# Kernel optimization log

Hardware: AMD Instinct MI355X
Metric: run time of the kernel (lower is better)

Reference implementation:

```python
import jax, jax.numpy as jnp
import numpy as np

N = 100000      # nodes
E = 3200000     # edges (avg degree 32)
IN = 256        # in_channels
OUT = 8         # out_channels
H1, C1 = 4, 4   # conv1: heads=4, out_channels=4 (concat -> 16)


def setup_inputs() -> dict:
    key = jax.random.key(0)
    ks = jax.random.split(key, 10)
    x = jax.random.normal(ks[0], (N, IN), jnp.float32)
    edge_index = jax.random.randint(ks[1], (2, E), 0, N, dtype=jnp.int64)

    def glorot(k, shape):
        fan_in = shape[0]
        return jax.random.normal(k, shape, jnp.float32) / np.float32(np.sqrt(fan_in))

    W1l = glorot(ks[2], (IN, H1 * C1))
    W1r = glorot(ks[3], (IN, H1 * C1))
    a1 = jax.random.normal(ks[4], (H1, C1), jnp.float32) / np.float32(np.sqrt(C1))
    b1 = jnp.zeros((H1 * C1,), jnp.float32)
    W2l = glorot(ks[5], (H1 * C1, OUT))
    W2r = glorot(ks[6], (H1 * C1, OUT))
    a2 = jax.random.normal(ks[7], (1, OUT), jnp.float32) / np.float32(np.sqrt(OUT))
    b2 = jnp.zeros((OUT,), jnp.float32)
    return {"x": x, "edge_index": edge_index, "W1l": W1l, "W1r": W1r, "a1": a1,
            "b1": b1, "W2l": W2l, "W2r": W2r, "a2": a2, "b2": b2}


def gatv2_conv(x, edge_index, Wl, Wr, att, bias, heads, ch, concat):
    # GATv2: e_ij = a^T LeakyReLU(Wl x_j + Wr x_i), softmax over incoming edges of i
    n = x.shape[0]
    src, dst = edge_index[0], edge_index[1]          # message flows src -> dst
    xl = (x @ Wl).reshape(n, heads, ch)              # [N,H,C] (source transform)
    xr = (x @ Wr).reshape(n, heads, ch)              # [N,H,C] (target transform)
    e = jax.nn.leaky_relu(xl[src] + xr[dst], 0.2)    # [E,H,C]
    logits = jnp.einsum('ehc,hc->eh', e, att)        # [E,H]
    # segment softmax over dst (stable: subtract per-target max)
    m = jax.ops.segment_max(logits, dst, num_segments=n)          # [N,H]
    ex = jnp.exp(logits - m[dst])                                  # [E,H]
    denom = jax.ops.segment_sum(ex, dst, num_segments=n)          # [N,H]
    alpha = ex / (denom[dst] + 1e-16)                              # [E,H]
    out = jax.ops.segment_sum(alpha[:, :, None] * xl[src], dst, num_segments=n)  # [N,H,C]
    out = out.reshape(n, heads * ch) if concat else out.mean(axis=1)
    return out + bias


def reference(x, edge_index, W1l, W1r, a1, b1, W2l, W2r, a2, b2):
    # eval mode: feature/attention dropout (p=0.6) are identity
    h = jax.nn.elu(gatv2_conv(x, edge_index, W1l, W1r, a1, b1, H1, C1, True))
    h = gatv2_conv(h, edge_index, W2l, W2r, a2, b2, 1, OUT, False)
    return jax.nn.sigmoid(h)
```

## Files before the change

kernel.cpp:

```cpp
#include <hip/hip_runtime.h>
#include <math.h>

#define NN 100000
#define NE 3200000
#define BW 512
#define BSH 9
#define NB 196
#define EPB_A 8192
#define NBLK_A ((NE + EPB_A - 1) / EPB_A)

__device__ __forceinline__ float lrelu(float v) { return v >= 0.f ? v : 0.2f * v; }


__global__ __launch_bounds__(256) void k_bhist(const int* __restrict__ dst,
                                               unsigned* __restrict__ btot) {
  __shared__ unsigned lh[NB];
  int tid = threadIdx.x;
  if (tid < NB) lh[tid] = 0;
  __syncthreads();
  int base = blockIdx.x * EPB_A;
  int end = min(base + EPB_A, NE);
  for (int e = base + tid * 4; e < end; e += 1024) {
    int4 d4 = *(const int4*)(dst + e);
    atomicAdd(&lh[((unsigned)d4.x) >> BSH], 1u);
    atomicAdd(&lh[((unsigned)d4.y) >> BSH], 1u);
    atomicAdd(&lh[((unsigned)d4.z) >> BSH], 1u);
    atomicAdd(&lh[((unsigned)d4.w) >> BSH], 1u);
  }
  __syncthreads();
  if (tid < NB && lh[tid]) atomicAdd(&btot[tid], lh[tid]);
}

__global__ __launch_bounds__(256) void k_bscan(const unsigned* __restrict__ btot,
    unsigned* __restrict__ bstart, unsigned* __restrict__ bcur) {
  __shared__ unsigned sm[256];
  int tid = threadIdx.x;
  unsigned v = (tid < NB) ? btot[tid] : 0;
  sm[tid] = v;
  __syncthreads();
  for (int off = 1; off < 256; off <<= 1) {
    unsigned u = (tid >= off) ? sm[tid - off] : 0;
    __syncthreads();
    sm[tid] += u;
    __syncthreads();
  }
  unsigned exc = sm[tid] - v;
  if (tid < NB) { bstart[tid] = exc; bcur[tid] = exc; }
  if (tid == NB - 1) bstart[NB] = sm[tid];
}

__global__ __launch_bounds__(256) void k_bin(const int* __restrict__ src,
    const int* __restrict__ dst, unsigned* __restrict__ bcur,
    unsigned* __restrict__ abuf) {
  __shared__ unsigned lh[NB], gb[NB], lcur[NB];
  int tid = threadIdx.x;
  if (tid < NB) lh[tid] = 0;
  __syncthreads();
  int base = blockIdx.x * EPB_A;
  int end = min(base + EPB_A, NE);
  for (int e = base + tid * 4; e < end; e += 1024) {
    int4 d4 = *(const int4*)(dst + e);
    atomicAdd(&lh[((unsigned)d4.x) >> BSH], 1u);
    atomicAdd(&lh[((unsigned)d4.y) >> BSH], 1u);
    atomicAdd(&lh[((unsigned)d4.z) >> BSH], 1u);
    atomicAdd(&lh[((unsigned)d4.w) >> BSH], 1u);
  }
  __syncthreads();
  if (tid < NB) {
    unsigned c = lh[tid];
    gb[tid] = c ? atomicAdd(&bcur[tid], c) : 0u;
    lcur[tid] = 0;
  }
  __syncthreads();
  for (int e = base + tid * 4; e < end; e += 1024) {
    int4 d4 = *(const int4*)(dst + e);
    int4 s4 = *(const int4*)(src + e);
    #pragma unroll
    for (int k = 0; k < 4; ++k) {
      unsigned d = (unsigned)(&d4.x)[k];
      unsigned s = (unsigned)(&s4.x)[k];
      unsigned b = d >> BSH;
      unsigned p = gb[b] + atomicAdd(&lcur[b], 1u);
      abuf[p] = ((d & (BW - 1)) << 17) | s;
    }
  }
}

__global__ __launch_bounds__(256) void k_bsort(const unsigned* __restrict__ bstart,
    const unsigned* __restrict__ abuf, int* __restrict__ rowstart,
    int* __restrict__ cnt, int* __restrict__ ssrc) {
  __shared__ unsigned lh[BW];
  __shared__ unsigned lcur[BW];
  __shared__ unsigned sm[256];
  int b = blockIdx.x, tid = threadIdx.x;
  unsigned s0 = bstart[b], s1 = bstart[b + 1];
  lh[tid] = 0; lh[tid + 256] = 0;
  __syncthreads();
  for (unsigned i = s0 + tid; i < s1; i += 256)
    atomicAdd(&lh[abuf[i] >> 17], 1u);
  __syncthreads();
  unsigned a0 = lh[2 * tid], a1 = lh[2 * tid + 1];
  sm[tid] = a0 + a1;
  __syncthreads();
  for (int off = 1; off < 256; off <<= 1) {
    unsigned u = (tid >= off) ? sm[tid - off] : 0;
    __syncthreads();
    sm[tid] += u;
    __syncthreads();
  }
  unsigned exc = sm[tid] - (a0 + a1);
  int node = b * BW + 2 * tid;
  if (node < NN)     { rowstart[node]     = s0 + exc;      cnt[node]     = a0; }
  if (node + 1 < NN) { rowstart[node + 1] = s0 + exc + a0; cnt[node + 1] = a1; }
  lcur[2 * tid] = exc;
  lcur[2 * tid + 1] = exc + a0;
  __syncthreads();
  for (unsigned i = s0 + tid; i < s1; i += 256) {
    unsigned v = abuf[i];
    unsigned p = s0 + atomicAdd(&lcur[v >> 17], 1u);
    ssrc[p] = (int)(v & 0x1FFFFu);
  }
}


__global__ __launch_bounds__(256) void k1_lin1(const float* __restrict__ x,
    const float* __restrict__ W1l, const float* __restrict__ W1r,
    float* __restrict__ xl1, float* __restrict__ xr1) {
  __shared__ float lw[256][32];
  int tid = threadIdx.x;
  for (int i = tid; i < 256 * 16; i += 256) {
    int k = i >> 4, c = i & 15;
    lw[k][c]      = W1l[i];
    lw[k][16 + c] = W1r[i];
  }
  __syncthreads();
  int row = blockIdx.x * 256 + tid;
  if (row >= NN) return;
  const float4* xr4 = (const float4*)(x + (size_t)row * 256);

  float acc[32];
  #pragma unroll
  for (int c = 0; c < 32; ++c) acc[c] = 0.f;

  float4 va = xr4[0], vb = xr4[1];
  for (int k4 = 0; k4 < 64; k4 += 2) {
    float4 vc = xr4[(k4 + 2) & 63];
    float4 vd = xr4[(k4 + 3) & 63];
    #pragma unroll
    for (int half = 0; half < 2; ++half) {
      float4 v = half ? vb : va;
      int kb = (k4 + half) * 4;
      #pragma unroll
      for (int kk = 0; kk < 4; ++kk) {
        float xk = (&v.x)[kk];
        const float4* wrow = (const float4*)&lw[kb + kk][0];
        #pragma unroll
        for (int q = 0; q < 8; ++q) {
          float4 w = wrow[q];
          acc[q * 4 + 0] = fmaf(xk, w.x, acc[q * 4 + 0]);
          acc[q * 4 + 1] = fmaf(xk, w.y, acc[q * 4 + 1]);
          acc[q * 4 + 2] = fmaf(xk, w.z, acc[q * 4 + 2]);
          acc[q * 4 + 3] = fmaf(xk, w.w, acc[q * 4 + 3]);
        }
      }
    }
    va = vc; vb = vd;
  }
  float4* ol = (float4*)(xl1 + (size_t)row * 16);
  float4* orr = (float4*)(xr1 + (size_t)row * 16);
  #pragma unroll
  for (int q = 0; q < 4; ++q) {
    ol[q]  = make_float4(acc[q*4+0], acc[q*4+1], acc[q*4+2], acc[q*4+3]);
    orr[q] = make_float4(acc[16+q*4+0], acc[16+q*4+1], acc[16+q*4+2], acc[16+q*4+3]);
  }
}


__global__ __launch_bounds__(256) void k_l1(const float* __restrict__ xl1,
    const float* __restrict__ xr1, const float* __restrict__ a1,
    const float* __restrict__ b1, const int* __restrict__ rowstart,
    const int* __restrict__ cnt, const int* __restrict__ ssrc,
    float* __restrict__ hbuf) {
  int tid = threadIdx.x;
  int i = (blockIdx.x * 256 + tid) >> 6;
  if (i >= NN) return;
  int lane = tid & 63;
  int j = lane >> 2, h = lane & 3;

  float4 xr = *(const float4*)(xr1 + (size_t)i * 16 + h * 4);
  float4 av = *(const float4*)(a1 + h * 4);
  int rs = rowstart[i], deg = cnt[i];

  float den = 0.f;
  float4 acc = make_float4(0.f, 0.f, 0.f, 0.f);

  for (int base = 0; base < deg; base += 16) {
    int jj = base + j;
    bool valid = jj < deg;
    int s = valid ? ssrc[rs + jj] : 0;
    float4 xl = *(const float4*)(xl1 + (size_t)s * 16 + h * 4);
    float lg = lrelu(xl.x + xr.x) * av.x + lrelu(xl.y + xr.y) * av.y +
               lrelu(xl.z + xr.z) * av.z + lrelu(xl.w + xr.w) * av.w;
    float p = valid ? __expf(lg) : 0.f;
    den += p;
    acc.x = fmaf(p, xl.x, acc.x);
    acc.y = fmaf(p, xl.y, acc.y);
    acc.z = fmaf(p, xl.z, acc.z);
    acc.w = fmaf(p, xl.w, acc.w);
  }
  #pragma unroll
  for (int st = 4; st <= 32; st <<= 1) {
    den   += __shfl_xor(den, st);
    acc.x += __shfl_xor(acc.x, st);
    acc.y += __shfl_xor(acc.y, st);
    acc.z += __shfl_xor(acc.z, st);
    acc.w += __shfl_xor(acc.w, st);
  }
  if (j == 0) {
    float inv = 1.f / (den + 1e-16f);
    float4 bv = *(const float4*)(b1 + h * 4);
    float v0 = fmaf(acc.x, inv, bv.x);
    float v1 = fmaf(acc.y, inv, bv.y);
    float v2 = fmaf(acc.z, inv, bv.z);
    float v3 = fmaf(acc.w, inv, bv.w);
    v0 = v0 > 0.f ? v0 : __expf(v0) - 1.f;
    v1 = v1 > 0.f ? v1 : __expf(v1) - 1.f;
    v2 = v2 > 0.f ? v2 : __expf(v2) - 1.f;
    v3 = v3 > 0.f ? v3 : __expf(v3) - 1.f;
    *(float4*)(hbuf + (size_t)i * 16 + h * 4) = make_float4(v0, v1, v2, v3);
  }
}


__global__ __launch_bounds__(256) void k5_mid(const float* __restrict__ hbuf,
    const float* __restrict__ W2l, const float* __restrict__ W2r,
    float* __restrict__ xl2, float* __restrict__ xr2) {
  __shared__ float w2[16][16];
  int tid = threadIdx.x;
  if (tid < 128) {
    int k = tid >> 3, c = tid & 7;
    w2[k][c]     = W2l[tid];
    w2[k][8 + c] = W2r[tid];
  }
  __syncthreads();
  int n = blockIdx.x * 256 + tid;
  if (n >= NN) return;
  float hh[16];
  const float4* hp = (const float4*)(hbuf + (size_t)n * 16);
  #pragma unroll
  for (int q = 0; q < 4; ++q) *(float4*)&hh[q * 4] = hp[q];
  float ol[8], orr[8];
  #pragma unroll
  for (int jq = 0; jq < 8; ++jq) { ol[jq] = 0.f; orr[jq] = 0.f; }
  #pragma unroll
  for (int k = 0; k < 16; ++k) {
    float hv = hh[k];
    #pragma unroll
    for (int jq = 0; jq < 8; ++jq) {
      ol[jq]  = fmaf(hv, w2[k][jq], ol[jq]);
      orr[jq] = fmaf(hv, w2[k][8 + jq], orr[jq]);
    }
  }
  *(float4*)(xl2 + (size_t)n * 8)     = make_float4(ol[0], ol[1], ol[2], ol[3]);
  *(float4*)(xl2 + (size_t)n * 8 + 4) = make_float4(ol[4], ol[5], ol[6], ol[7]);
  *(float4*)(xr2 + (size_t)n * 8)     = make_float4(orr[0], orr[1], orr[2], orr[3]);
  *(float4*)(xr2 + (size_t)n * 8 + 4) = make_float4(orr[4], orr[5], orr[6], orr[7]);
}


__global__ __launch_bounds__(256) void k_l2(const float* __restrict__ xl2,
    const float* __restrict__ xr2, const float* __restrict__ a2,
    const float* __restrict__ b2, const int* __restrict__ rowstart,
    const int* __restrict__ cnt, const int* __restrict__ ssrc,
    float* __restrict__ out) {
  int tid = threadIdx.x;
  int i = (blockIdx.x * 256 + tid) >> 6;
  if (i >= NN) return;
  int lane = tid & 63;
  int j = lane >> 3, c = lane & 7;

  float xrc = xr2[(size_t)i * 8 + c];
  float avc = a2[c];
  int rs = rowstart[i], deg = cnt[i];

  float den = 0.f, accc = 0.f;
  for (int base = 0; base < deg; base += 8) {
    int jj = base + j;
    bool valid = jj < deg;
    int s = valid ? ssrc[rs + jj] : 0;
    float xlc = xl2[(size_t)s * 8 + c];
    float lg = lrelu(xlc + xrc) * avc;
    lg += __shfl_xor(lg, 1);
    lg += __shfl_xor(lg, 2);
    lg += __shfl_xor(lg, 4);
    float p = valid ? __expf(lg) : 0.f;
    den += p;
    accc = fmaf(p, xlc, accc);
  }
  #pragma unroll
  for (int st = 8; st <= 32; st <<= 1) {
    den  += __shfl_xor(den, st);
    accc += __shfl_xor(accc, st);
  }
  if (j == 0) {
    float v = accc / (den + 1e-16f) + b2[c];
    out[(size_t)i * 8 + c] = 1.f / (1.f + __expf(-v));
  }
}


extern "C" void kernel_launch(void* const* d_in, const int* in_sizes, int n_in,
                              void* d_out, int out_size, void* d_ws, size_t ws_size,
                              hipStream_t stream) {
  const float* x   = (const float*)d_in[0];
  const int*   ei  = (const int*)d_in[1];
  const float* W1l = (const float*)d_in[2];
  const float* W1r = (const float*)d_in[3];
  const float* a1  = (const float*)d_in[4];
  const float* b1  = (const float*)d_in[5];
  const float* W2l = (const float*)d_in[6];
  const float* W2r = (const float*)d_in[7];
  const float* a2  = (const float*)d_in[8];
  const float* b2  = (const float*)d_in[9];
  const int* src = ei;
  const int* dst = ei + NE;

  char* ws = (char*)d_ws;
  size_t off = 0;
  auto alloc = [&](size_t bytes) { void* p = (void*)(ws + off); off += (bytes + 255) & ~(size_t)255; return p; };
  unsigned* btot   = (unsigned*)alloc((size_t)NB * 4);
  unsigned* bstart = (unsigned*)alloc((size_t)(NB + 1) * 4);
  unsigned* bcur   = (unsigned*)alloc((size_t)NB * 4);
  int*      rowstart = (int*)alloc((size_t)NN * 4);
  int*      cnt      = (int*)alloc((size_t)NN * 4);
  int*      ssrc     = (int*)alloc((size_t)NE * 4);
  char*     bigbase  = (char*)alloc((size_t)NN * 16 * 4 * 2);
  unsigned* abuf = (unsigned*)bigbase;
  float*    xl1  = (float*)bigbase;
  float*    xr1  = (float*)(bigbase + (size_t)NN * 16 * 4);
  float*    xl2  = (float*)alloc((size_t)NN * 8 * 4);
  float*    xr2  = (float*)alloc((size_t)NN * 8 * 4);
  float*    hbuf = (float*)alloc((size_t)NN * 16 * 4);

  hipMemsetAsync(btot, 0, (size_t)NB * 4, stream);

  k_bhist<<<NBLK_A, 256, 0, stream>>>(dst, btot);
  k_bscan<<<1, 256, 0, stream>>>(btot, bstart, bcur);
  k_bin  <<<NBLK_A, 256, 0, stream>>>(src, dst, bcur, abuf);
  k_bsort<<<NB, 256, 0, stream>>>(bstart, abuf, rowstart, cnt, ssrc);

  k1_lin1<<<(NN + 255) / 256, 256, 0, stream>>>(x, W1l, W1r, xl1, xr1);

  int gw = (NN * 64 + 255) / 256;
  k_l1<<<gw, 256, 0, stream>>>(xl1, xr1, a1, b1, rowstart, cnt, ssrc, hbuf);
  k5_mid<<<(NN + 255) / 256, 256, 0, stream>>>(hbuf, W2l, W2r, xl2, xr2);
  k_l2<<<gw, 256, 0, stream>>>(xl2, xr2, a2, b2, rowstart, cnt, ssrc, (float*)d_out);
}
```

Before: 412.8 us.

## Replace full CSR sort with coarse bucketing and per-bucket shared-memory atomic aggregation

Drops the second-level per-node sort (k_bsort) and instead buckets edges by destination into 128-node bins. A per-block histogram table gives deterministic write offsets without a second histogram pass. Both attention layers now process a bucket per block, accumulating softmax numerators and denominators with shared-memory float atomics, and layer 1 is fused with the second linear transform. The softmax max-subtraction is omitted, as before. Risks include shared atomic contention, loss of summation determinism, and limited parallelism with only 782 blocks.

```diff
diff --git a/kernel.cpp b/kernel.cpp
--- a/kernel.cpp
+++ b/kernel.cpp
@@ -3,23 +3,23 @@
 
 #define NN 100000
 #define NE 3200000
-#define BW 512
-#define BSH 9
-#define NB 196
-#define EPB_A 8192
-#define NBLK_A ((NE + EPB_A - 1) / EPB_A)
+#define BW 128
+#define BSH 7
+#define NB 782
+#define EPB 8192
+#define NBLKH ((NE + EPB - 1) / EPB)
 
 __device__ __forceinline__ float lrelu(float v) { return v >= 0.f ? v : 0.2f * v; }
 
 
 __global__ __launch_bounds__(256) void k_bhist(const int* __restrict__ dst,
-                                               unsigned* __restrict__ btot) {
+    unsigned* __restrict__ btot, unsigned* __restrict__ hcnt) {
   __shared__ unsigned lh[NB];
   int tid = threadIdx.x;
-  if (tid < NB) lh[tid] = 0;
-  __syncthreads();
-  int base = blockIdx.x * EPB_A;
-  int end = min(base + EPB_A, NE);
+  for (int i = tid; i < NB; i += 256) lh[i] = 0;
+  __syncthreads();
+  int base = blockIdx.x * EPB;
+  int end = min(base + EPB, NE);
   for (int e = base + tid * 4; e < end; e += 1024) {
     int4 d4 = *(const int4*)(dst + e);
     atomicAdd(&lh[((unsigned)d4.x) >> BSH], 1u);
@@ -28,50 +28,64 @@
     atomicAdd(&lh[((unsigned)d4.w) >> BSH], 1u);
   }
   __syncthreads();
-  if (tid < NB && lh[tid]) atomicAdd(&btot[tid], lh[tid]);
+  unsigned* row = hcnt + (size_t)blockIdx.x * NB;
+  for (int i = tid; i < NB; i += 256) {
+    unsigned c = lh[i];
+    row[i] = c;
+    if (c) atomicAdd(&btot[i], c);
+  }
 }
 
 __global__ __launch_bounds__(256) void k_bscan(const unsigned* __restrict__ btot,
-    unsigned* __restrict__ bstart, unsigned* __restrict__ bcur) {
+                                               unsigned* __restrict__ bstart) {
   __shared__ unsigned sm[256];
   int tid = threadIdx.x;
-  unsigned v = (tid < NB) ? btot[tid] : 0;
-  sm[tid] = v;
+  int base = tid * 4;
+  unsigned c[4];
+  #pragma unroll
+  for (int k = 0; k < 4; ++k) c[k] = (base + k < NB) ? btot[base + k] : 0u;
+  unsigned s = c[0] + c[1] + c[2] + c[3];
+  sm[tid] = s;
   __syncthreads();
   for (int off = 1; off < 256; off <<= 1) {
-    unsigned u = (tid >= off) ? sm[tid - off] : 0;
+    unsigned u = (tid >= off) ? sm[tid - off] : 0u;
     __syncthreads();
     sm[tid] += u;
     __syncthreads();
   }
-  unsigned exc = sm[tid] - v;
-  if (tid < NB) { bstart[tid] = exc; bcur[tid] = exc; }
-  if (tid == NB - 1) bstart[NB] = sm[tid];
+  unsigned run = sm[tid] - s;
+  #pragma unroll
+  for (int k = 0; k < 4; ++k) {
+    if (base + k < NB) bstart[base + k] = run;
+    run += c[k];
+  }
+  if (tid == 255) bstart[NB] = sm[255];
+}
+
+__global__ __launch_bounds__(256) void k_boff(const unsigned* __restrict__ bstart,
+                                              unsigned* __restrict__ hcnt) {
+  int b = blockIdx.x * 256 + threadIdx.x;
+  if (b >= NB) return;
+  unsigned run = bstart[b];
+  for (int blk = 0; blk < NBLKH; ++blk) {
+    size_t idx = (size_t)blk * NB + b;
+    unsigned c = hcnt[idx];
+    hcnt[idx] = run;
+    run += c;
+  }
 }
 
 __global__ __launch_bounds__(256) void k_bin(const int* __restrict__ src,
-    const int* __restrict__ dst, unsigned* __restrict__ bcur,
+    const int* __restrict__ dst, const unsigned* __restrict__ hcnt,
     unsigned* __restrict__ abuf) {
-  __shared__ unsigned lh[NB], gb[NB], lcur[NB];
-  int tid = threadIdx.x;
-  if (tid < NB) lh[tid] = 0;
-  __syncthreads();
-  int base = blockIdx.x * EPB_A;
-  int end = min(base + EPB_A, NE);
-  for (int e = base + tid * 4; e < end; e += 1024) {
-    int4 d4 = *(const int4*)(dst + e);
-    atomicAdd(&lh[((unsigned)d4.x) >> BSH], 1u);
-    atomicAdd(&lh[((unsigned)d4.y) >> BSH], 1u);
-    atomicAdd(&lh[((unsigned)d4.z) >> BSH], 1u);
-    atomicAdd(&lh[((unsigned)d4.w) >> BSH], 1u);
-  }
-  __syncthreads();
-  if (tid < NB) {
-    unsigned c = lh[tid];
-    gb[tid] = c ? atomicAdd(&bcur[tid], c) : 0u;
-    lcur[tid] = 0;
-  }
-  __syncthreads();
+  __shared__ unsigned gb[NB];
+  __shared__ unsigned lcur[NB];
+  int tid = threadIdx.x;
+  const unsigned* row = hcnt + (size_t)blockIdx.x * NB;
+  for (int i = tid; i < NB; i += 256) { gb[i] = row[i]; lcur[i] = 0; }
+  __syncthreads();
+  int base = blockIdx.x * EPB;
+  int end = min(base + EPB, NE);
   for (int e = base + tid * 4; e < end; e += 1024) {
     int4 d4 = *(const int4*)(dst + e);
     int4 s4 = *(const int4*)(src + e);
@@ -83,42 +97,6 @@
       unsigned p = gb[b] + atomicAdd(&lcur[b], 1u);
       abuf[p] = ((d & (BW - 1)) << 17) | s;
     }
-  }
-}
-
-__global__ __launch_bounds__(256) void k_bsort(const unsigned* __restrict__ bstart,
-    const unsigned* __restrict__ abuf, int* __restrict__ rowstart,
-    int* __restrict__ cnt, int* __restrict__ ssrc) {
-  __shared__ unsigned lh[BW];
-  __shared__ unsigned lcur[BW];
-  __shared__ unsigned sm[256];
-  int b = blockIdx.x, tid = threadIdx.x;
-  unsigned s0 = bstart[b], s1 = bstart[b + 1];
-  lh[tid] = 0; lh[tid + 256] = 0;
-  __syncthreads();
-  for (unsigned i = s0 + tid; i < s1; i += 256)
-    atomicAdd(&lh[abuf[i] >> 17], 1u);
-  __syncthreads();
-  unsigned a0 = lh[2 * tid], a1 = lh[2 * tid + 1];
-  sm[tid] = a0 + a1;
-  __syncthreads();
-  for (int off = 1; off < 256; off <<= 1) {
-    unsigned u = (tid >= off) ? sm[tid - off] : 0;
-    __syncthreads();
-    sm[tid] += u;
-    __syncthreads();
-  }
-  unsigned exc = sm[tid] - (a0 + a1);
-  int node = b * BW + 2 * tid;
-  if (node < NN)     { rowstart[node]     = s0 + exc;      cnt[node]     = a0; }
-  if (node + 1 < NN) { rowstart[node + 1] = s0 + exc + a0; cnt[node + 1] = a1; }
-  lcur[2 * tid] = exc;
-  lcur[2 * tid + 1] = exc + a0;
-  __syncthreads();
-  for (unsigned i = s0 + tid; i < s1; i += 256) {
-    unsigned v = abuf[i];
-    unsigned p = s0 + atomicAdd(&lcur[v >> 17], 1u);
-    ssrc[p] = (int)(v & 0x1FFFFu);
   }
 }
 
@@ -176,135 +154,144 @@
 }
 
 
-__global__ __launch_bounds__(256) void k_l1(const float* __restrict__ xl1,
+__global__ __launch_bounds__(256) void k_l1b(const float* __restrict__ xl1,
     const float* __restrict__ xr1, const float* __restrict__ a1,
-    const float* __restrict__ b1, const int* __restrict__ rowstart,
-    const int* __restrict__ cnt, const int* __restrict__ ssrc,
-    float* __restrict__ hbuf) {
-  int tid = threadIdx.x;
-  int i = (blockIdx.x * 256 + tid) >> 6;
-  if (i >= NN) return;
-  int lane = tid & 63;
-  int j = lane >> 2, h = lane & 3;
-
-  float4 xr = *(const float4*)(xr1 + (size_t)i * 16 + h * 4);
-  float4 av = *(const float4*)(a1 + h * 4);
-  int rs = rowstart[i], deg = cnt[i];
-
-  float den = 0.f;
-  float4 acc = make_float4(0.f, 0.f, 0.f, 0.f);
-
-  for (int base = 0; base < deg; base += 16) {
-    int jj = base + j;
-    bool valid = jj < deg;
-    int s = valid ? ssrc[rs + jj] : 0;
-    float4 xl = *(const float4*)(xl1 + (size_t)s * 16 + h * 4);
-    float lg = lrelu(xl.x + xr.x) * av.x + lrelu(xl.y + xr.y) * av.y +
-               lrelu(xl.z + xr.z) * av.z + lrelu(xl.w + xr.w) * av.w;
-    float p = valid ? __expf(lg) : 0.f;
-    den += p;
-    acc.x = fmaf(p, xl.x, acc.x);
-    acc.y = fmaf(p, xl.y, acc.y);
-    acc.z = fmaf(p, xl.z, acc.z);
-    acc.w = fmaf(p, xl.w, acc.w);
-  }
-  #pragma unroll
-  for (int st = 4; st <= 32; st <<= 1) {
-    den   += __shfl_xor(den, st);
-    acc.x += __shfl_xor(acc.x, st);
-    acc.y += __shfl_xor(acc.y, st);
-    acc.z += __shfl_xor(acc.z, st);
-    acc.w += __shfl_xor(acc.w, st);
-  }
-  if (j == 0) {
-    float inv = 1.f / (den + 1e-16f);
-    float4 bv = *(const float4*)(b1 + h * 4);
-    float v0 = fmaf(acc.x, inv, bv.x);
-    float v1 = fmaf(acc.y, inv, bv.y);
-    float v2 = fmaf(acc.z, inv, bv.z);
-    float v3 = fmaf(acc.w, inv, bv.w);
-    v0 = v0 > 0.f ? v0 : __expf(v0) - 1.f;
-    v1 = v1 > 0.f ? v1 : __expf(v1) - 1.f;
-    v2 = v2 > 0.f ? v2 : __expf(v2) - 1.f;
-    v3 = v3 > 0.f ? v3 : __expf(v3) - 1.f;
-    *(float4*)(hbuf + (size_t)i * 16 + h * 4) = make_float4(v0, v1, v2, v3);
-  }
-}
-
-
-__global__ __launch_bounds__(256) void k5_mid(const float* __restrict__ hbuf,
-    const float* __restrict__ W2l, const float* __restrict__ W2r,
+    const float* __restrict__ b1, const float* __restrict__ W2l,
+    const float* __restrict__ W2r, const unsigned* __restrict__ bstart,
+    const unsigned* __restrict__ abuf,
     float* __restrict__ xl2, float* __restrict__ xr2) {
+  __shared__ float accs[16][BW];
+  __shared__ float dens[4][BW];
   __shared__ float w2[16][16];
   int tid = threadIdx.x;
+  int b = blockIdx.x;
+  for (int i = tid; i < 16 * BW; i += 256) accs[i >> BSH][i & (BW - 1)] = 0.f;
+  for (int i = tid; i < 4 * BW; i += 256) dens[i >> BSH][i & (BW - 1)] = 0.f;
   if (tid < 128) {
     int k = tid >> 3, c = tid & 7;
     w2[k][c]     = W2l[tid];
     w2[k][8 + c] = W2r[tid];
   }
   __syncthreads();
-  int n = blockIdx.x * 256 + tid;
-  if (n >= NN) return;
-  float hh[16];
-  const float4* hp = (const float4*)(hbuf + (size_t)n * 16);
-  #pragma unroll
-  for (int q = 0; q < 4; ++q) *(float4*)&hh[q * 4] = hp[q];
-  float ol[8], orr[8];
-  #pragma unroll
-  for (int jq = 0; jq < 8; ++jq) { ol[jq] = 0.f; orr[jq] = 0.f; }
-  #pragma unroll
-  for (int k = 0; k < 16; ++k) {
-    float hv = hh[k];
+
+  unsigned s0 = bstart[b], s1 = bstart[b + 1];
+  int node0 = b * BW;
+  float a1r[16];
+  #pragma unroll
+  for (int c = 0; c < 16; ++c) a1r[c] = a1[c];
+
+  for (unsigned e = s0 + tid; e < s1; e += 256) {
+    unsigned v = abuf[e];
+    unsigned s = v & 0x1FFFFu;
+    unsigned dloc = (v >> 17) & (BW - 1);
+    const float4* xlp = (const float4*)(xl1 + (size_t)s * 16);
+    const float4* xrp = (const float4*)(xr1 + (size_t)(node0 + dloc) * 16);
     #pragma unroll
-    for (int jq = 0; jq < 8; ++jq) {
-      ol[jq]  = fmaf(hv, w2[k][jq], ol[jq]);
-      orr[jq] = fmaf(hv, w2[k][8 + jq], orr[jq]);
-    }
-  }
-  *(float4*)(xl2 + (size_t)n * 8)     = make_float4(ol[0], ol[1], ol[2], ol[3]);
-  *(float4*)(xl2 + (size_t)n * 8 + 4) = make_float4(ol[4], ol[5], ol[6], ol[7]);
-  *(float4*)(xr2 + (size_t)n * 8)     = make_float4(orr[0], orr[1], orr[2], orr[3]);
-  *(float4*)(xr2 + (size_t)n * 8 + 4) = make_float4(orr[4], orr[5], orr[6], orr[7]);
-}
-
-
-__global__ __launch_bounds__(256) void k_l2(const float* __restrict__ xl2,
+    for (int h = 0; h < 4; ++h) {
+      float4 xl = xlp[h];
+      float4 xr = xrp[h];
+      float lg = lrelu(xl.x + xr.x) * a1r[h*4+0] + lrelu(xl.y + xr.y) * a1r[h*4+1]
+               + lrelu(xl.z + xr.z) * a1r[h*4+2] + lrelu(xl.w + xr.w) * a1r[h*4+3];
+      float p = __expf(lg);
+      atomicAdd(&dens[h][dloc], p);
+      atomicAdd(&accs[h*4+0][dloc], p * xl.x);
+      atomicAdd(&accs[h*4+1][dloc], p * xl.y);
+      atomicAdd(&accs[h*4+2][dloc], p * xl.z);
+      atomicAdd(&accs[h*4+3][dloc], p * xl.w);
+    }
+  }
+  __syncthreads();
+
+  if (tid < BW) {
+    int n = node0 + tid;
+    if (n < NN) {
+      float hh[16];
+      #pragma unroll
+      for (int h = 0; h < 4; ++h) {
+        float inv = 1.f / (dens[h][tid] + 1e-16f);
+        #pragma unroll
+        for (int c = 0; c < 4; ++c) {
+          float v = fmaf(accs[h*4+c][tid], inv, b1[h*4+c]);
+          hh[h*4+c] = v > 0.f ? v : __expf(v) - 1.f;
+        }
+      }
+      float ol[8], orr[8];
+      #pragma unroll
+      for (int j = 0; j < 8; ++j) { ol[j] = 0.f; orr[j] = 0.f; }
+      #pragma unroll
+      for (int k = 0; k < 16; ++k) {
+        float hv = hh[k];
+        #pragma unroll
+        for (int j = 0; j < 8; ++j) {
+          ol[j]  = fmaf(hv, w2[k][j], ol[j]);
+          orr[j] = fmaf(hv, w2[k][8 + j], orr[j]);
+        }
+      }
+      *(float4*)(xl2 + (size_t)n * 8)     = make_float4(ol[0], ol[1], ol[2], ol[3]);
+      *(float4*)(xl2 + (size_t)n * 8 + 4) = make_float4(ol[4], ol[5], ol[6], ol[7]);
+      *(float4*)(xr2 + (size_t)n * 8)     = make_float4(orr[0], orr[1], orr[2], orr[3]);
+      *(float4*)(xr2 + (size_t)n * 8 + 4) = make_float4(orr[4], orr[5], orr[6], orr[7]);
+    }
+  }
+}
+
+
+__global__ __launch_bounds__(256) void k_l2b(const float* __restrict__ xl2,
     const float* __restrict__ xr2, const float* __restrict__ a2,
-    const float* __restrict__ b2, const int* __restrict__ rowstart,
-    const int* __restrict__ cnt, const int* __restrict__ ssrc,
-    float* __restrict__ out) {
-  int tid = threadIdx.x;
-  int i = (blockIdx.x * 256 + tid) >> 6;
-  if (i >= NN) return;
-  int lane = tid & 63;
-  int j = lane >> 3, c = lane & 7;
-
-  float xrc = xr2[(size_t)i * 8 + c];
-  float avc = a2[c];
-  int rs = rowstart[i], deg = cnt[i];
-
-  float den = 0.f, accc = 0.f;
-  for (int base = 0; base < deg; base += 8) {
-    int jj = base + j;
-    bool valid = jj < deg;
-    int s = valid ? ssrc[rs + jj] : 0;
-    float xlc = xl2[(size_t)s * 8 + c];
-    float lg = lrelu(xlc + xrc) * avc;
-    lg += __shfl_xor(lg, 1);
-    lg += __shfl_xor(lg, 2);
-    lg += __shfl_xor(lg, 4);
-    float p = valid ? __expf(lg) : 0.f;
-    den += p;
-    accc = fmaf(p, xlc, accc);
-  }
-  #pragma unroll
-  for (int st = 8; st <= 32; st <<= 1) {
-    den  += __shfl_xor(den, st);
-    accc += __shfl_xor(accc, st);
-  }
-  if (j == 0) {
-    float v = accc / (den + 1e-16f) + b2[c];
-    out[(size_t)i * 8 + c] = 1.f / (1.f + __expf(-v));
+    const float* __restrict__ b2, const unsigned* __restrict__ bstart,
+    const unsigned* __restrict__ abuf, float* __restrict__ out) {
+  __shared__ float accs[8][BW];
+  __shared__ float dens[BW];
+  int tid = threadIdx.x;
+  int b = blockIdx.x;
+  for (int i = tid; i < 8 * BW; i += 256) accs[i >> BSH][i & (BW - 1)] = 0.f;
+  if (tid < BW) dens[tid] = 0.f;
+  __syncthreads();
+
+  unsigned s0 = bstart[b], s1 = bstart[b + 1];
+  int node0 = b * BW;
+  float a2r[8];
+  #pragma unroll
+  for (int c = 0; c < 8; ++c) a2r[c] = a2[c];
+
+  for (unsigned e = s0 + tid; e < s1; e += 256) {
+    unsigned v = abuf[e];
+    unsigned s = v & 0x1FFFFu;
+    unsigned dloc = (v >> 17) & (BW - 1);
+    const float4* xlp = (const float4*)(xl2 + (size_t)s * 8);
+    const float4* xrp = (const float4*)(xr2 + (size_t)(node0 + dloc) * 8);
+    float4 l0 = xlp[0], l1v = xlp[1];
+    float4 r0 = xrp[0], r1v = xrp[1];
+    float lg = lrelu(l0.x + r0.x) * a2r[0] + lrelu(l0.y + r0.y) * a2r[1]
+             + lrelu(l0.z + r0.z) * a2r[2] + lrelu(l0.w + r0.w) * a2r[3]
+             + lrelu(l1v.x + r1v.x) * a2r[4] + lrelu(l1v.y + r1v.y) * a2r[5]
+             + lrelu(l1v.z + r1v.z) * a2r[6] + lrelu(l1v.w + r1v.w) * a2r[7];
+    float p = __expf(lg);
+    atomicAdd(&dens[dloc], p);
+    atomicAdd(&accs[0][dloc], p * l0.x);
+    atomicAdd(&accs[1][dloc], p * l0.y);
+    atomicAdd(&accs[2][dloc], p * l0.z);
+    atomicAdd(&accs[3][dloc], p * l0.w);
+    atomicAdd(&accs[4][dloc], p * l1v.x);
+    atomicAdd(&accs[5][dloc], p * l1v.y);
+    atomicAdd(&accs[6][dloc], p * l1v.z);
+    atomicAdd(&accs[7][dloc], p * l1v.w);
+  }
+  __syncthreads();
+
+  if (tid < BW) {
+    int n = node0 + tid;
+    if (n < NN) {
+      float inv = 1.f / (dens[tid] + 1e-16f);
+      float o[8];
+      #pragma unroll
+      for (int c = 0; c < 8; ++c) {
+        float v = fmaf(accs[c][tid], inv, b2[c]);
+        o[c] = 1.f / (1.f + __expf(-v));
+      }
+      *(float4*)(out + (size_t)n * 8)     = make_float4(o[0], o[1], o[2], o[3]);
+      *(float4*)(out + (size_t)n * 8 + 4) = make_float4(o[4], o[5], o[6], o[7]);
+    }
   }
 }
 
@@ -330,29 +317,22 @@
   auto alloc = [&](size_t bytes) { void* p = (void*)(ws + off); off += (bytes + 255) & ~(size_t)255; return p; };
   unsigned* btot   = (unsigned*)alloc((size_t)NB * 4);
   unsigned* bstart = (unsigned*)alloc((size_t)(NB + 1) * 4);
-  unsigned* bcur   = (unsigned*)alloc((size_t)NB * 4);
-  int*      rowstart = (int*)alloc((size_t)NN * 4);
-  int*      cnt      = (int*)alloc((size_t)NN * 4);
-  int*      ssrc     = (int*)alloc((size_t)NE * 4);
-  char*     bigbase  = (char*)alloc((size_t)NN * 16 * 4 * 2);
-  unsigned* abuf = (unsigned*)bigbase;
-  float*    xl1  = (float*)bigbase;
-  float*    xr1  = (float*)(bigbase + (size_t)NN * 16 * 4);
-  float*    xl2  = (float*)alloc((size_t)NN * 8 * 4);
-  float*    xr2  = (float*)alloc((size_t)NN * 8 * 4);
-  float*    hbuf = (float*)alloc((size_t)NN * 16 * 4);
+  unsigned* hcnt   = (unsigned*)alloc((size_t)NBLKH * NB * 4);
+  unsigned* abuf   = (unsigned*)alloc((size_t)NE * 4);
+  float*    xl1    = (float*)alloc((size_t)NN * 16 * 4);
+  float*    xr1    = (float*)alloc((size_t)NN * 16 * 4);
+  float*    xl2    = (float*)alloc((size_t)NN * 8 * 4);
+  float*    xr2    = (float*)alloc((size_t)NN * 8 * 4);
 
   hipMemsetAsync(btot, 0, (size_t)NB * 4, stream);
 
-  k_bhist<<<NBLK_A, 256, 0, stream>>>(dst, btot);
-  k_bscan<<<1, 256, 0, stream>>>(btot, bstart, bcur);
-  k_bin  <<<NBLK_A, 256, 0, stream>>>(src, dst, bcur, abuf);
-  k_bsort<<<NB, 256, 0, stream>>>(bstart, abuf, rowstart, cnt, ssrc);
+  k_bhist<<<NBLKH, 256, 0, stream>>>(dst, btot, hcnt);
+  k_bscan<<<1, 256, 0, stream>>>(btot, bstart);
+  k_boff <<<(NB + 255) / 256, 256, 0, stream>>>(bstart, hcnt);
+  k_bin  <<<NBLKH, 256, 0, stream>>>(src, dst, hcnt, abuf);
 
   k1_lin1<<<(NN + 255) / 256, 256, 0, stream>>>(x, W1l, W1r, xl1, xr1);
 
-  int gw = (NN * 64 + 255) / 256;
-  k_l1<<<gw, 256, 0, stream>>>(xl1, xr1, a1, b1, rowstart, cnt, ssrc, hbuf);
-  k5_mid<<<(NN + 255) / 256, 256, 0, stream>>>(hbuf, W2l, W2r, xl2, xr2);
-  k_l2<<<gw, 256, 0, stream>>>(xl2, xr2, a2, b2, rowstart, cnt, ssrc, (float*)d_out);
-}
+  k_l1b<<<NB, 256, 0, stream>>>(xl1, xr1, a1, b1, W2l, W2r, bstart, abuf, xl2, xr2);
+  k_l2b<<<NB, 256, 0, stream>>>(xl2, xr2, a2, b2, bstart, abuf, (float*)d_out);
+}
```

Result: slower. 888.7 us (+115.3%).
